# Performance work log

Measured on AMD Instinct MI355X. Metric: run time of the kernel, lower is better.

Reference implementation:

```python
import jax, jax.numpy as jnp
import numpy as np

H = 256          # h_dim
SEQ_LEN = 10     # max history length
B = 2048         # number of queries with non-empty history
N = 327680       # total flattened neighbors across all (query, timestep) segments
NUM_SEG = B * SEQ_LEN
NUM_ENT = 20000
NUM_REL = 200


def setup_inputs() -> dict:
    key = jax.random.key(0)
    ks = jax.random.split(key, 9)
    s = jax.random.randint(ks[0], (B,), 0, NUM_ENT)
    r = jax.random.randint(ks[1], (B,), 0, NUM_REL)
    nbr_ids = jax.random.randint(ks[2], (N,), 0, NUM_ENT)
    seg_ids = jnp.sort(jax.random.randint(ks[3], (N,), 0, NUM_SEG))
    ent_embeds = jax.random.normal(ks[4], (NUM_ENT, H), dtype=jnp.float32)
    rel_embeds = jax.random.normal(ks[5], (NUM_REL, H), dtype=jnp.float32)
    W_attn = jax.random.normal(ks[6], (3 * H, H), dtype=jnp.float32) * 0.05
    b_attn = jax.random.normal(ks[7], (H,), dtype=jnp.float32) * 0.05
    v_s = jax.random.normal(ks[8], (H, 1), dtype=jnp.float32) * 0.05
    return {"s": s, "r": r, "nbr_ids": nbr_ids, "seg_ids": seg_ids,
            "ent_embeds": ent_embeds, "rel_embeds": rel_embeds,
            "W_attn": W_attn, "b_attn": b_attn, "v_s": v_s}


def reference(s, r, nbr_ids, seg_ids, ent_embeds, rel_embeds, W_attn, b_attn, v_s):
    # Per-neighbor gathers. Each neighbor belongs to segment seg = q*SEQ_LEN + t.
    q = seg_ids // SEQ_LEN                              # query index per neighbor [N]
    em = ent_embeds[nbr_ids]                            # [N, H] neighbor embeddings
    s_emb = ent_embeds[s]                               # [B, H]
    r_emb = rel_embeds[r]                               # [B, H]
    ss = s_emb[q]                                       # [N, H]
    rr = r_emb[q]                                       # [N, H]
    # Score: tanh(Linear(3H -> H)) @ v_s  -> scalar per neighbor
    x = jnp.concatenate([em, ss, rr], axis=1)           # [N, 3H]
    scores = (jnp.tanh(x @ W_attn + b_attn) @ v_s)[:, 0]  # [N]
    # Segment softmax over neighbors within each (query, timestep) segment.
    m = jax.ops.segment_max(scores, seg_ids, num_segments=NUM_SEG)  # [S]
    e = jnp.exp(scores - m[seg_ids])                    # [N]
    denom = jax.ops.segment_sum(e, seg_ids, num_segments=NUM_SEG)   # [S]
    w = e / denom[seg_ids]                              # [N]
    # Weighted sum of neighbor embeddings per segment (scatter-reduce).
    agg = jax.ops.segment_sum(w[:, None] * em, seg_ids, num_segments=NUM_SEG)  # [S, H]
    counts = jax.ops.segment_sum(jnp.ones_like(scores), seg_ids, num_segments=NUM_SEG)
    mask = (counts > 0).astype(em.dtype).reshape(B, SEQ_LEN, 1)     # present timesteps
    agg = agg.reshape(B, SEQ_LEN, H)
    ss_t = jnp.broadcast_to(s_emb[:, None, :], (B, SEQ_LEN, H))
    rr_t = jnp.broadcast_to(r_emb[:, None, :], (B, SEQ_LEN, H))
    # Padded [B, SEQ_LEN, 3H] sequence tensor (rows for empty segments are zero,
    # matching the torch code's zero-initialized padded tensor). Dropout p=0.0.
    out = jnp.concatenate([agg, ss_t, rr_t], axis=2) * mask
    return out
```

## Files before the change

kernel.cpp:

```cpp
#include <hip/hip_runtime.h>
#include <hip/hip_bf16.h>

#define H 256
#define SEQ 10

typedef __attribute__((ext_vector_type(8))) short bf16x8;
typedef __attribute__((ext_vector_type(4))) short bf16x4;
typedef __attribute__((ext_vector_type(4))) float f32x4;

__device__ __forceinline__ unsigned short f2bf(float x) {
    union { float f; unsigned u; } v; v.f = x;
    unsigned r = v.u + 0x7fff + ((v.u >> 16) & 1);
    return (unsigned short)(r >> 16);
}
__device__ __forceinline__ float bf2f(unsigned short b) {
    union { unsigned u; float f; } v; v.u = ((unsigned)b) << 16;
    return v.f;
}
__device__ __forceinline__ float fast_tanh(float x) {
    float t = __expf(2.f * x);
    return 1.f - 2.f * __builtin_amdgcn_rcpf(t + 1.f);
}

__global__ void conv_ent_kernel(const float* __restrict__ ent,
                                unsigned short* __restrict__ comb, int n) {
    int g0 = (blockIdx.x * blockDim.x + threadIdx.x) * 8;
    if (g0 >= n) return;
    float4 a = *reinterpret_cast<const float4*>(ent + g0);
    float4 b = *reinterpret_cast<const float4*>(ent + g0 + 4);
    bf16x8 o;
    o[0] = (short)f2bf(a.x); o[1] = (short)f2bf(a.y);
    o[2] = (short)f2bf(a.z); o[3] = (short)f2bf(a.w);
    o[4] = (short)f2bf(b.x); o[5] = (short)f2bf(b.y);
    o[6] = (short)f2bf(b.z); o[7] = (short)f2bf(b.w);
    int e = g0 >> 8, i = g0 & 255;
    *reinterpret_cast<bf16x8*>(comb + (size_t)e * 512 + 256 + i) = o;
}

__global__ void prep_Wt_kernel(const float* __restrict__ W,
                               unsigned short* __restrict__ Wt) {
    int idx = blockIdx.x * blockDim.x + threadIdx.x;
    if (idx >= H * 3 * H) return;
    int n = idx / (3 * H), k = idx % (3 * H);
    Wt[idx] = f2bf(W[k * H + n]);
}

__global__ void seg_start_kernel(const int* __restrict__ seg_ids,
                                 int* __restrict__ seg_start, int n, int num_seg) {
    int j = blockIdx.x * blockDim.x + threadIdx.x;
    if (j >= n) return;
    int cur = seg_ids[j];
    int prev = (j == 0) ? -1 : seg_ids[j - 1];
    for (int s2 = prev + 1; s2 <= cur; s2++) seg_start[s2] = j;
    if (j == n - 1)
        for (int s2 = cur + 1; s2 <= num_seg; s2++) seg_start[s2] = n;
}

__global__ void gemm_bf16_kernel(const unsigned short* __restrict__ Abf,
                                 const int* __restrict__ sidx,
                                 const int* __restrict__ ridx,
                                 const float* __restrict__ ent,
                                 const float* __restrict__ rel,
                                 const unsigned short* __restrict__ Wt,
                                 const float* __restrict__ bias,
                                 unsigned short* __restrict__ out,
                                 int M, int K, int k0, int mode, int lda, int ldo) {
    __shared__ unsigned short As[64][40];
    __shared__ unsigned short Bs[64][40];
    int t = threadIdx.x;
    int m0 = blockIdx.x * 64;
    int n0 = blockIdx.y * 64;
    int sr = t >> 2;
    int sc = (t & 3) * 8;
    int wave = t >> 6, lane = t & 63;
    int lr = lane & 15, lg = lane >> 4;

    f32x4 acc[4] = {{0.f, 0.f, 0.f, 0.f}, {0.f, 0.f, 0.f, 0.f},
                    {0.f, 0.f, 0.f, 0.f}, {0.f, 0.f, 0.f, 0.f}};

    for (int kk = 0; kk < K; kk += 32) {
        bf16x8 av = {};
        int gm = m0 + sr;
        if (mode == 0) {
            if (gm < M)
                av = *reinterpret_cast<const bf16x8*>(Abf + (size_t)gm * lda + kk + sc);
        } else {
            int k = kk + sc;
            const float* src = (k < H) ? (ent + (size_t)sidx[gm] * H + k)
                                       : (rel + (size_t)ridx[gm] * H + (k - H));
            float4 f0 = *reinterpret_cast<const float4*>(src);
            float4 f1 = *reinterpret_cast<const float4*>(src + 4);
            av[0] = (short)f2bf(f0.x); av[1] = (short)f2bf(f0.y);
            av[2] = (short)f2bf(f0.z); av[3] = (short)f2bf(f0.w);
            av[4] = (short)f2bf(f1.x); av[5] = (short)f2bf(f1.y);
            av[6] = (short)f2bf(f1.z); av[7] = (short)f2bf(f1.w);
        }
        *reinterpret_cast<bf16x8*>(&As[sr][sc]) = av;
        bf16x8 bv = *reinterpret_cast<const bf16x8*>(
            Wt + (size_t)(n0 + sr) * (3 * H) + k0 + kk + sc);
        *reinterpret_cast<bf16x8*>(&Bs[sr][sc]) = bv;
        __syncthreads();

        bf16x8 bfr = *reinterpret_cast<const bf16x8*>(&Bs[wave * 16 + lr][lg * 8]);
#pragma unroll
        for (int mf = 0; mf < 4; mf++) {
            bf16x8 afr = *reinterpret_cast<const bf16x8*>(&As[mf * 16 + lr][lg * 8]);
            acc[mf] = __builtin_amdgcn_mfma_f32_16x16x32_bf16(afr, bfr, acc[mf], 0, 0, 0);
        }
        __syncthreads();
    }

    int col = n0 + wave * 16 + lr;
    float bv = bias ? bias[col] : 0.f;
#pragma unroll
    for (int mf = 0; mf < 4; mf++) {
#pragma unroll
        for (int rr = 0; rr < 4; rr++) {
            int row = m0 + mf * 16 + lg * 4 + rr;
            if (row < M)
                out[(size_t)row * ldo + col] = f2bf(acc[mf][rr] + bv);
        }
    }
}

__global__ void fused_agg_kernel(const int* __restrict__ nbr_ids,
                                 const int* __restrict__ seg_start,
                                 const unsigned short* __restrict__ comb,
                                 const unsigned short* __restrict__ qpartbf,
                                 const float* __restrict__ v_s,
                                 const float* __restrict__ ent_embeds,
                                 const float* __restrict__ rel_embeds,
                                 const int* __restrict__ s,
                                 const int* __restrict__ r,
                                 float* __restrict__ out, int num_seg) {
    int seg = blockIdx.x * 4 + (threadIdx.x >> 6);
    if (seg >= num_seg) return;
    int lane = threadIdx.x & 63;
    int b = seg / SEQ;
    int start = seg_start[seg], end = seg_start[seg + 1];
    float* orow = out + (size_t)seg * (3 * H);
    int c4 = lane * 4;

    if (start == end) {
        float4 z = {0.f, 0.f, 0.f, 0.f};
        *reinterpret_cast<float4*>(orow + c4) = z;
        *reinterpret_cast<float4*>(orow + H + c4) = z;
        *reinterpret_cast<float4*>(orow + 2 * H + c4) = z;
        return;
    }

    int g = lane >> 4, li = lane & 15;
    int cb = li * 16;

    float qv[16], vv[16];
    {
        bf16x8 qa = *reinterpret_cast<const bf16x8*>(qpartbf + (size_t)b * H + cb);
        bf16x8 qb = *reinterpret_cast<const bf16x8*>(qpartbf + (size_t)b * H + cb + 8);
#pragma unroll
        for (int k = 0; k < 8; k++) {
            qv[k] = bf2f((unsigned short)qa[k]);
            qv[8 + k] = bf2f((unsigned short)qb[k]);
        }
        const float4* vp = reinterpret_cast<const float4*>(v_s + cb);
#pragma unroll
        for (int k = 0; k < 4; k++) {
            float4 tv = vp[k];
            vv[4 * k + 0] = tv.x; vv[4 * k + 1] = tv.y;
            vv[4 * k + 2] = tv.z; vv[4 * k + 3] = tv.w;
        }
    }

    float acc[16];
#pragma unroll
    for (int k = 0; k < 16; k++) acc[k] = 0.f;
    float lpart = 0.f;

    int cc = end - start;
    int nitm = (cc + 3) >> 2;
    for (int ji = 0; ji < nitm; ji++) {
        int j = 4 * ji + g;
        if (j < cc) {
            int nbr = nbr_ids[start + j];
            const unsigned short* row = comb + (size_t)nbr * 512 + cb;
            bf16x8 p0 = *reinterpret_cast<const bf16x8*>(row);
            bf16x8 p1 = *reinterpret_cast<const bf16x8*>(row + 8);
            bf16x8 e0 = *reinterpret_cast<const bf16x8*>(row + 256);
            bf16x8 e1 = *reinterpret_cast<const bf16x8*>(row + 264);
            float s16 = 0.f;
#pragma unroll
            for (int k = 0; k < 8; k++) {
                s16 += fast_tanh(bf2f((unsigned short)p0[k]) + qv[k]) * vv[k];
                s16 += fast_tanh(bf2f((unsigned short)p1[k]) + qv[8 + k]) * vv[8 + k];
            }
            s16 += __shfl_xor(s16, 1);
            s16 += __shfl_xor(s16, 2);
            s16 += __shfl_xor(s16, 4);
            s16 += __shfl_xor(s16, 8);
            float e = __expf(s16);
            lpart += e;
#pragma unroll
            for (int k = 0; k < 8; k++) {
                acc[k] += e * bf2f((unsigned short)e0[k]);
                acc[8 + k] += e * bf2f((unsigned short)e1[k]);
            }
        }
    }

    lpart += __shfl_xor(lpart, 16);
    lpart += __shfl_xor(lpart, 32);
#pragma unroll
    for (int k = 0; k < 16; k++) {
        acc[k] += __shfl_xor(acc[k], 16);
        acc[k] += __shfl_xor(acc[k], 32);
    }
    float invl = 1.f / lpart;

    float4 o;
#pragma unroll
    for (int k = 0; k < 4; k++) {
        float v0 = acc[k], v1 = acc[4 + k], v2 = acc[8 + k], v3 = acc[12 + k];
        float pick = (g == 0) ? v0 : (g == 1) ? v1 : (g == 2) ? v2 : v3;
        if (k == 0) o.x = pick * invl;
        else if (k == 1) o.y = pick * invl;
        else if (k == 2) o.z = pick * invl;
        else o.w = pick * invl;
    }
    *reinterpret_cast<float4*>(orow + cb + 4 * g) = o;
    *reinterpret_cast<float4*>(orow + H + c4) =
        *reinterpret_cast<const float4*>(ent_embeds + (size_t)s[b] * H + c4);
    *reinterpret_cast<float4*>(orow + 2 * H + c4) =
        *reinterpret_cast<const float4*>(rel_embeds + (size_t)r[b] * H + c4);
}

extern "C" void kernel_launch(void* const* d_in, const int* in_sizes, int n_in,
                              void* d_out, int out_size, void* d_ws, size_t ws_size,
                              hipStream_t stream) {
    const int* s = (const int*)d_in[0];
    const int* r = (const int*)d_in[1];
    const int* nbr_ids = (const int*)d_in[2];
    const int* seg_ids = (const int*)d_in[3];
    const float* ent_embeds = (const float*)d_in[4];
    const float* rel_embeds = (const float*)d_in[5];
    const float* W_attn = (const float*)d_in[6];
    const float* b_attn = (const float*)d_in[7];
    const float* v_s = (const float*)d_in[8];
    float* out = (float*)d_out;

    int B = in_sizes[0];
    int N = in_sizes[2];
    int num_ent = in_sizes[4] / H;
    int num_seg = B * SEQ;

    char* ws = (char*)d_ws;
    unsigned short* comb = (unsigned short*)ws;
    unsigned short* Wt = comb + (size_t)num_ent * 512;
    unsigned short* qpartbf = Wt + (size_t)H * 3 * H;
    int* seg_start = (int*)(qpartbf + (size_t)B * H);

    int n_ent_el = num_ent * H;
    conv_ent_kernel<<<(n_ent_el / 8 + 255) / 256, 256, 0, stream>>>(ent_embeds, comb, n_ent_el);
    prep_Wt_kernel<<<(H * 3 * H + 255) / 256, 256, 0, stream>>>(W_attn, Wt);
    seg_start_kernel<<<(N + 255) / 256, 256, 0, stream>>>(seg_ids, seg_start, N, num_seg);

    dim3 g1((num_ent + 63) / 64, H / 64);
    gemm_bf16_kernel<<<g1, 256, 0, stream>>>(comb + 256, nullptr, nullptr, nullptr, nullptr,
                                             Wt, nullptr, comb, num_ent, H, 0, 0, 512, 512);
    dim3 g2(B / 64, H / 64);
    gemm_bf16_kernel<<<g2, 256, 0, stream>>>(nullptr, s, r, ent_embeds, rel_embeds,
                                             Wt, b_attn, qpartbf, B, 2 * H, H, 1, 0, H);

    fused_agg_kernel<<<(num_seg + 3) / 4, 256, 0, stream>>>(
        nbr_ids, seg_start, comb, qpartbf, v_s,
        ent_embeds, rel_embeds, s, r, out, num_seg);
}
```

Before: 105.4 us.

## Fuse entity bf16 conversion into GEMM, prefetch neighbor rows, shrink agg blocks

Removes the separate entity fp32->bf16 conversion kernel. The first GEMM now reads fp32 entities directly and, in its n0==0 blocks, writes the bf16 copy into the combined table. The aggregation loop software-prefetches the next neighbor's row and masks out-of-range items instead of branching. It also uses exp2-based tanh/exp and 128-thread blocks with 2 segments each. These changes save a launch and a memory pass and hide gather latency, at the cost of redundant clamped loads and more registers.

Result: no change. 103.9 us (-1.5%).

```diff
diff --git a/kernel.cpp b/kernel.cpp
--- a/kernel.cpp
+++ b/kernel.cpp
@@ -17,24 +17,12 @@
     union { unsigned u; float f; } v; v.u = ((unsigned)b) << 16;
     return v.f;
 }
+__device__ __forceinline__ float fexp2(float x) {
+    return __builtin_amdgcn_exp2f(x);
+}
 __device__ __forceinline__ float fast_tanh(float x) {
-    float t = __expf(2.f * x);
+    float t = fexp2(x * 2.885390082f);
     return 1.f - 2.f * __builtin_amdgcn_rcpf(t + 1.f);
-}
-
-__global__ void conv_ent_kernel(const float* __restrict__ ent,
-                                unsigned short* __restrict__ comb, int n) {
-    int g0 = (blockIdx.x * blockDim.x + threadIdx.x) * 8;
-    if (g0 >= n) return;
-    float4 a = *reinterpret_cast<const float4*>(ent + g0);
-    float4 b = *reinterpret_cast<const float4*>(ent + g0 + 4);
-    bf16x8 o;
-    o[0] = (short)f2bf(a.x); o[1] = (short)f2bf(a.y);
-    o[2] = (short)f2bf(a.z); o[3] = (short)f2bf(a.w);
-    o[4] = (short)f2bf(b.x); o[5] = (short)f2bf(b.y);
-    o[6] = (short)f2bf(b.z); o[7] = (short)f2bf(b.w);
-    int e = g0 >> 8, i = g0 & 255;
-    *reinterpret_cast<bf16x8*>(comb + (size_t)e * 512 + 256 + i) = o;
 }
 
 __global__ void prep_Wt_kernel(const float* __restrict__ W,
@@ -56,7 +44,7 @@
         for (int s2 = cur + 1; s2 <= num_seg; s2++) seg_start[s2] = n;
 }
 
-__global__ void gemm_bf16_kernel(const unsigned short* __restrict__ Abf,
+__global__ void gemm_bf16_kernel(const float* __restrict__ entf,
                                  const int* __restrict__ sidx,
                                  const int* __restrict__ ridx,
                                  const float* __restrict__ ent,
@@ -64,7 +52,8 @@
                                  const unsigned short* __restrict__ Wt,
                                  const float* __restrict__ bias,
                                  unsigned short* __restrict__ out,
-                                 int M, int K, int k0, int mode, int lda, int ldo) {
+                                 unsigned short* __restrict__ em_out,
+                                 int M, int K, int k0, int mode, int ldo) {
     __shared__ unsigned short As[64][40];
     __shared__ unsigned short Bs[64][40];
     int t = threadIdx.x;
@@ -81,19 +70,23 @@
     for (int kk = 0; kk < K; kk += 32) {
         bf16x8 av = {};
         int gm = m0 + sr;
-        if (mode == 0) {
-            if (gm < M)
-                av = *reinterpret_cast<const bf16x8*>(Abf + (size_t)gm * lda + kk + sc);
-        } else {
-            int k = kk + sc;
-            const float* src = (k < H) ? (ent + (size_t)sidx[gm] * H + k)
-                                       : (rel + (size_t)ridx[gm] * H + (k - H));
+        if (gm < M) {
+            const float* src;
+            if (mode == 0) {
+                src = entf + (size_t)gm * H + kk + sc;
+            } else {
+                int k = kk + sc;
+                src = (k < H) ? (ent + (size_t)sidx[gm] * H + k)
+                              : (rel + (size_t)ridx[gm] * H + (k - H));
+            }
             float4 f0 = *reinterpret_cast<const float4*>(src);
             float4 f1 = *reinterpret_cast<const float4*>(src + 4);
             av[0] = (short)f2bf(f0.x); av[1] = (short)f2bf(f0.y);
             av[2] = (short)f2bf(f0.z); av[3] = (short)f2bf(f0.w);
             av[4] = (short)f2bf(f1.x); av[5] = (short)f2bf(f1.y);
             av[6] = (short)f2bf(f1.z); av[7] = (short)f2bf(f1.w);
+            if (mode == 0 && em_out && n0 == 0)
+                *reinterpret_cast<bf16x8*>(em_out + (size_t)gm * 512 + 256 + kk + sc) = av;
         }
         *reinterpret_cast<bf16x8*>(&As[sr][sc]) = av;
         bf16x8 bv = *reinterpret_cast<const bf16x8*>(
@@ -123,17 +116,18 @@
     }
 }
 
-__global__ void fused_agg_kernel(const int* __restrict__ nbr_ids,
-                                 const int* __restrict__ seg_start,
-                                 const unsigned short* __restrict__ comb,
-                                 const unsigned short* __restrict__ qpartbf,
-                                 const float* __restrict__ v_s,
-                                 const float* __restrict__ ent_embeds,
-                                 const float* __restrict__ rel_embeds,
-                                 const int* __restrict__ s,
-                                 const int* __restrict__ r,
-                                 float* __restrict__ out, int num_seg) {
-    int seg = blockIdx.x * 4 + (threadIdx.x >> 6);
+__global__ void __launch_bounds__(128)
+fused_agg_kernel(const int* __restrict__ nbr_ids,
+                 const int* __restrict__ seg_start,
+                 const unsigned short* __restrict__ comb,
+                 const unsigned short* __restrict__ qpartbf,
+                 const float* __restrict__ v_s,
+                 const float* __restrict__ ent_embeds,
+                 const float* __restrict__ rel_embeds,
+                 const int* __restrict__ s,
+                 const int* __restrict__ r,
+                 float* __restrict__ out, int num_seg) {
+    int seg = blockIdx.x * 2 + (threadIdx.x >> 6);
     if (seg >= num_seg) return;
     int lane = threadIdx.x & 63;
     int b = seg / SEQ;
@@ -177,33 +171,41 @@
 
     int cc = end - start;
     int nitm = (cc + 3) >> 2;
+
+    int j0 = min(g, cc - 1);
+    const unsigned short* row = comb + (size_t)nbr_ids[start + j0] * 512 + cb;
+    bf16x8 p0 = *reinterpret_cast<const bf16x8*>(row);
+    bf16x8 p1 = *reinterpret_cast<const bf16x8*>(row + 8);
+    bf16x8 e0 = *reinterpret_cast<const bf16x8*>(row + 256);
+    bf16x8 e1 = *reinterpret_cast<const bf16x8*>(row + 264);
+
     for (int ji = 0; ji < nitm; ji++) {
-        int j = 4 * ji + g;
-        if (j < cc) {
-            int nbr = nbr_ids[start + j];
-            const unsigned short* row = comb + (size_t)nbr * 512 + cb;
-            bf16x8 p0 = *reinterpret_cast<const bf16x8*>(row);
-            bf16x8 p1 = *reinterpret_cast<const bf16x8*>(row + 8);
-            bf16x8 e0 = *reinterpret_cast<const bf16x8*>(row + 256);
-            bf16x8 e1 = *reinterpret_cast<const bf16x8*>(row + 264);
-            float s16 = 0.f;
-#pragma unroll
-            for (int k = 0; k < 8; k++) {
-                s16 += fast_tanh(bf2f((unsigned short)p0[k]) + qv[k]) * vv[k];
-                s16 += fast_tanh(bf2f((unsigned short)p1[k]) + qv[8 + k]) * vv[8 + k];
-            }
-            s16 += __shfl_xor(s16, 1);
-            s16 += __shfl_xor(s16, 2);
-            s16 += __shfl_xor(s16, 4);
-            s16 += __shfl_xor(s16, 8);
-            float e = __expf(s16);
-            lpart += e;
-#pragma unroll
-            for (int k = 0; k < 8; k++) {
-                acc[k] += e * bf2f((unsigned short)e0[k]);
-                acc[8 + k] += e * bf2f((unsigned short)e1[k]);
-            }
-        }
+        int jn = min(4 * (ji + 1) + g, cc - 1);
+        const unsigned short* rown = comb + (size_t)nbr_ids[start + jn] * 512 + cb;
+        bf16x8 p0n = *reinterpret_cast<const bf16x8*>(rown);
+        bf16x8 p1n = *reinterpret_cast<const bf16x8*>(rown + 8);
+        bf16x8 e0n = *reinterpret_cast<const bf16x8*>(rown + 256);
+        bf16x8 e1n = *reinterpret_cast<const bf16x8*>(rown + 264);
+
+        float s16 = 0.f;
+#pragma unroll
+        for (int k = 0; k < 8; k++) {
+            s16 += fast_tanh(bf2f((unsigned short)p0[k]) + qv[k]) * vv[k];
+            s16 += fast_tanh(bf2f((unsigned short)p1[k]) + qv[8 + k]) * vv[8 + k];
+        }
+        s16 += __shfl_xor(s16, 1);
+        s16 += __shfl_xor(s16, 2);
+        s16 += __shfl_xor(s16, 4);
+        s16 += __shfl_xor(s16, 8);
+        float e = fexp2(s16 * 1.4426950408889634f);
+        e = (4 * ji + g < cc) ? e : 0.f;
+        lpart += e;
+#pragma unroll
+        for (int k = 0; k < 8; k++) {
+            acc[k] += e * bf2f((unsigned short)e0[k]);
+            acc[8 + k] += e * bf2f((unsigned short)e1[k]);
+        }
+        p0 = p0n; p1 = p1n; e0 = e0n; e1 = e1n;
     }
 
     lpart += __shfl_xor(lpart, 16);
@@ -257,19 +259,19 @@
     unsigned short* qpartbf = Wt + (size_t)H * 3 * H;
     int* seg_start = (int*)(qpartbf + (size_t)B * H);
 
-    int n_ent_el = num_ent * H;
-    conv_ent_kernel<<<(n_ent_el / 8 + 255) / 256, 256, 0, stream>>>(ent_embeds, comb, n_ent_el);
     prep_Wt_kernel<<<(H * 3 * H + 255) / 256, 256, 0, stream>>>(W_attn, Wt);
     seg_start_kernel<<<(N + 255) / 256, 256, 0, stream>>>(seg_ids, seg_start, N, num_seg);
 
     dim3 g1((num_ent + 63) / 64, H / 64);
-    gemm_bf16_kernel<<<g1, 256, 0, stream>>>(comb + 256, nullptr, nullptr, nullptr, nullptr,
-                                             Wt, nullptr, comb, num_ent, H, 0, 0, 512, 512);
+    gemm_bf16_kernel<<<g1, 256, 0, stream>>>(ent_embeds, nullptr, nullptr, nullptr, nullptr,
+                                             Wt, nullptr, comb, comb,
+                                             num_ent, H, 0, 0, 512);
     dim3 g2(B / 64, H / 64);
     gemm_bf16_kernel<<<g2, 256, 0, stream>>>(nullptr, s, r, ent_embeds, rel_embeds,
-                                             Wt, b_attn, qpartbf, B, 2 * H, H, 1, 0, H);
-
-    fused_agg_kernel<<<(num_seg + 3) / 4, 256, 0, stream>>>(
+                                             Wt, b_attn, qpartbf, nullptr,
+                                             B, 2 * H, H, 1, H);
+
+    fused_agg_kernel<<<(num_seg + 1) / 2, 128, 0, stream>>>(
         nbr_ids, seg_start, comb, qpartbf, v_s,
         ent_embeds, rel_embeds, s, r, out, num_seg);
 }
```
